# Optimization experiments

Measured on AMD Instinct MI355X. Metric: run time of the kernel, lower is better.

## Reference

```python
import jax, jax.numpy as jnp
import numpy as np

HIDDEN = 1024
N_HEADS = 16
HEAD_DIM = HIDDEN // N_HEADS


def setup_inputs() -> dict:
    key = jax.random.key(0)
    ks = jax.random.split(key, 7)
    b, l, m = 4, 1024, 1024
    q = jax.random.normal(ks[0], (b, l, HIDDEN), dtype=jnp.float32)
    k = jax.random.normal(ks[1], (b, m, HIDDEN), dtype=jnp.float32)
    v = jax.random.normal(ks[2], (b, m, HIDDEN), dtype=jnp.float32)
    s = 1.0 / np.sqrt(HIDDEN)
    w_q = jax.random.normal(ks[3], (HIDDEN, HIDDEN), dtype=jnp.float32) * s
    w_k = jax.random.normal(ks[4], (HIDDEN, HIDDEN), dtype=jnp.float32) * s
    w_v = jax.random.normal(ks[5], (HIDDEN, HIDDEN), dtype=jnp.float32) * s
    w_o = jax.random.normal(ks[6], (HIDDEN, HIDDEN), dtype=jnp.float32) * s
    return {"q": q, "k": k, "v": v, "w_q": w_q, "w_k": w_k, "w_v": w_v, "w_o": w_o}


def reference(q, k, v, w_q, w_k, w_v, w_o):
    b, l, _ = q.shape
    _, m, _ = k.shape
    # Linear (bias=False): y = x @ W^T
    qp = q @ w_q.T
    kp = k @ w_k.T
    vp = v @ w_v.T  # projected but unused downstream (faithful to original bug)
    # Faithful non-standard split: hidden -> (head_dim, n_heads)
    qh = qp.reshape(b, l, HEAD_DIM, N_HEADS)
    kh = kp.reshape(b, m, HEAD_DIM, N_HEADS)
    # attn over K, scaled, softmax over m (dim=2)
    scores = jnp.einsum('bldn,bmdn->blmn', qh, kh) / np.sqrt(HEAD_DIM)
    attn = jax.nn.softmax(scores, axis=2)
    # dropout is identity in eval mode
    # NOTE: original attends over K (not V) — reproduced faithfully
    x = jnp.einsum('blmn,bmdn->bldn', attn, kh)
    x = x.reshape(b, l, HIDDEN)  # 'b l d n -> b l (d n)'
    return x @ w_o.T
```

## Files before the change

kernel.cpp:

```cpp
#include <hip/hip_runtime.h>
#include <hip/hip_bf16.h>
#include <stdint.h>
#include <math.h>


typedef __bf16 bf16;
typedef __bf16 bf16x8 __attribute__((ext_vector_type(8)));
typedef float  f32x4  __attribute__((ext_vector_type(4)));

__device__ __forceinline__ void async_load16(const void* g, void* l) {
  __builtin_amdgcn_global_load_lds((__attribute__((address_space(1))) void*)g,
                                   (__attribute__((address_space(3))) void*)l,
                                   16, 0, 0);
}

__device__ __forceinline__ float load_canon(const void* src, int i, int fl) {
  float f = fl ? ((const float*)src)[i] : (float)((const bf16*)src)[i];
  return fminf(fmaxf(f, -1024.f), 1024.f);
}

__global__ void __launch_bounds__(256)
canon_all(const void* __restrict__ q_raw, const void* __restrict__ k_raw,
          const void* __restrict__ wq_raw, const void* __restrict__ wk_raw,
          const void* __restrict__ wo_raw,
          bf16* __restrict__ q_c, bf16* __restrict__ k_c,
          bf16* __restrict__ wq_c, bf16* __restrict__ wk_c,
          bf16* __restrict__ wo_p, int* __restrict__ flag) {
  __shared__ int smax[4];
  const int tid = threadIdx.x;
  {
    int e = (((const unsigned short*)q_raw)[tid] >> 7) & 0xFF;
#pragma unroll
    for (int off = 1; off <= 32; off <<= 1) {
      int o = __shfl_xor(e, off);
      e = o > e ? o : e;
    }
    if ((tid & 63) == 0) smax[tid >> 6] = e;
  }
  __syncthreads();
  int m01 = smax[0] > smax[1] ? smax[0] : smax[1];
  int m23 = smax[2] > smax[3] ? smax[2] : smax[3];
  const int fl = ((m01 > m23 ? m01 : m23) >= 140) ? 1 : 0;

  const int blk = blockIdx.x;
  if (blk == 0 && tid == 0) *flag = fl;

  if (blk < 4096) {
    const void* src = blk < 2048 ? q_raw : k_raw;
    bf16* dst = blk < 2048 ? q_c : k_c;
    int i = (blk & 2047) * 2048 + tid * 8;
    bf16x8 v;
#pragma unroll
    for (int j = 0; j < 8; ++j) v[j] = (bf16)load_canon(src, i + j, fl);
    *(bf16x8*)(dst + i) = v;
  } else if (blk < 5120) {
    const void* src = blk < 4608 ? wq_raw : wk_raw;
    bf16* dst = blk < 4608 ? wq_c : wk_c;
    int i = ((blk - 4096) & 511) * 2048 + tid * 8;
    bf16x8 v;
#pragma unroll
    for (int j = 0; j < 8; ++j) v[j] = (bf16)load_canon(src, i + j, fl);
    *(bf16x8*)(dst + i) = v;
  } else {
    int i = (blk - 5120) * 2048 + tid * 8;
    int o = i >> 10, h0 = i & 1023;
#pragma unroll
    for (int j = 0; j < 8; ++j) {
      int h = h0 + j;
      int kp = ((h & 15) << 6) | (h >> 4);
      wo_p[o * 1024 + kp] = (bf16)load_canon(wo_raw, i + j, fl);
    }
  }
}

__global__ void __launch_bounds__(256, 2)
qk_gemm(const bf16* __restrict__ q_c, const bf16* __restrict__ wq_c,
        const bf16* __restrict__ k_c, const bf16* __restrict__ wk_c,
        bf16* __restrict__ qh, bf16* __restrict__ kh, bf16* __restrict__ khT,
        float cs) {
  __shared__ bf16 sA[128 * 64];
  __shared__ bf16 sB[128 * 64];
  __shared__ bf16 epi[128 * 134];

  const int z = blockIdx.z;
  const bf16* A = z ? k_c : q_c;
  const bf16* W = z ? wk_c : wq_c;
  const float scale = z ? 1.0f : cs;
  bf16* out0 = z ? kh : qh;

  const int tid  = threadIdx.x;
  const int lane = tid & 63;
  const int wave = tid >> 6;
  const int q4   = lane >> 4;
  const int c16  = lane & 15;
  const int wm   = wave >> 1;
  const int wn   = wave & 1;

  const int lin    = blockIdx.x + 8 * blockIdx.y;
  const int rowBlk = (lin & 31) * 128;
  const int colBlk = (lin >> 5) * 128;

  int ar[4], ag[4];
#pragma unroll
  for (int i = 0; i < 4; ++i) {
    int s = tid + 256 * i;
    ar[i] = s >> 3;
    ag[i] = (tid & 7) ^ (ar[i] & 7);
  }
  const bf16* gA[4];
  const bf16* gB[4];
  bf16 *lA[4], *lB[4];
#pragma unroll
  for (int i = 0; i < 4; ++i) {
    gA[i] = A + (size_t)(rowBlk + ar[i]) * 1024 + ag[i] * 8;
    gB[i] = W + (size_t)(colBlk + ar[i]) * 1024 + ag[i] * 8;
    lA[i] = sA + (tid + 256 * i) * 8;
    lB[i] = sB + (tid + 256 * i) * 8;
  }

  f32x4 acc[4][4] = {};

  for (int kk = 0; kk < 1024; kk += 64) {
    __syncthreads();
#pragma unroll
    for (int i = 0; i < 4; ++i) async_load16(gA[i] + kk, lA[i]);
#pragma unroll
    for (int i = 0; i < 4; ++i) async_load16(gB[i] + kk, lB[i]);
    __builtin_amdgcn_s_waitcnt(0);
    __syncthreads();

    bf16x8 af[2][4], bfr[2][4];
#pragma unroll
    for (int ks = 0; ks < 2; ++ks) {
#pragma unroll
      for (int mt = 0; mt < 4; ++mt) {
        int row = wm * 64 + mt * 16 + c16;
        af[ks][mt] = *(const bf16x8*)(sA + row * 64 +
                       (((ks * 4 + q4) ^ (row & 7)) * 8));
      }
#pragma unroll
      for (int nt = 0; nt < 4; ++nt) {
        int row = wn * 64 + nt * 16 + c16;
        bfr[ks][nt] = *(const bf16x8*)(sB + row * 64 +
                       (((ks * 4 + q4) ^ (row & 7)) * 8));
      }
    }
#pragma unroll
    for (int ks = 0; ks < 2; ++ks)
#pragma unroll
      for (int mt = 0; mt < 4; ++mt)
#pragma unroll
        for (int nt = 0; nt < 4; ++nt)
          acc[mt][nt] = __builtin_amdgcn_mfma_f32_16x16x32_bf16(
              af[ks][mt], bfr[ks][nt], acc[mt][nt], 0, 0, 0);
  }

  __syncthreads();
#pragma unroll
  for (int mt = 0; mt < 4; ++mt)
#pragma unroll
    for (int nt = 0; nt < 4; ++nt)
#pragma unroll
      for (int r = 0; r < 4; ++r) {
        int m_t = wm * 64 + mt * 16 + q4 * 4 + r;
        int h_t = wn * 64 + nt * 16 + c16;
        epi[m_t * 134 + h_t] = (bf16)(acc[mt][nt][r] * scale);
      }
  __syncthreads();

  const int bb    = rowBlk >> 10;
  const int mbase = rowBlk & 1023;
  const int dg0   = colBlk >> 4;

  {
    int n = tid >> 4;
#pragma unroll
    for (int i = 0; i < 8; ++i) {
      int m_t = (tid & 15) + i * 16;
      bf16x8 v;
#pragma unroll
      for (int dt = 0; dt < 8; ++dt) v[dt] = epi[m_t * 134 + dt * 16 + n];
      *(bf16x8*)(out0 + ((size_t)(bb * 16 + n) * 1024 + mbase + m_t) * 64 + dg0) = v;
    }
  }
  if (z) {
    int h_t = tid >> 1, half = tid & 1;
    int n = h_t & 15, dt = h_t >> 4;
    size_t base = ((size_t)(bb * 16 + n) * 64 + dg0 + dt) * 1024 + mbase + half * 64;
#pragma unroll
    for (int c = 0; c < 8; ++c) {
      bf16x8 v;
#pragma unroll
      for (int j = 0; j < 8; ++j) v[j] = epi[(half * 64 + c * 8 + j) * 134 + h_t];
      *(bf16x8*)(khT + base + c * 8) = v;
    }
  }
}

__global__ void __launch_bounds__(256, 2)
o_gemm(const bf16* __restrict__ A, const bf16* __restrict__ W,
       bf16* __restrict__ out0, float* __restrict__ outf,
       const int* __restrict__ flag) {
  __shared__ bf16 sA[128 * 64];
  __shared__ bf16 sB[64 * 64];

  const int tid  = threadIdx.x;
  const int lane = tid & 63;
  const int wave = tid >> 6;
  const int q4   = lane >> 4;
  const int c16  = lane & 15;
  const int wm   = wave >> 1;
  const int wn   = wave & 1;

  const int lin    = blockIdx.x + 16 * blockIdx.y;
  const int rowBlk = (lin & 31) * 128;
  const int colBlk = (lin >> 5) * 64;

  int ar[4], ag[4];
#pragma unroll
  for (int i = 0; i < 4; ++i) {
    int s = tid + 256 * i;
    ar[i] = s >> 3;
    ag[i] = (tid & 7) ^ (ar[i] & 7);
  }
  const bf16* gA[4];
  bf16* lA[4];
#pragma unroll
  for (int i = 0; i < 4; ++i) {
    gA[i] = A + (size_t)(rowBlk + ar[i]) * 1024 + ag[i] * 8;
    lA[i] = sA + (tid + 256 * i) * 8;
  }
  const bf16* gB[2];
  bf16* lB[2];
#pragma unroll
  for (int i = 0; i < 2; ++i) {
    int s = tid + 256 * i;
    int br = s >> 3, bg = (tid & 7) ^ (br & 7);
    gB[i] = W + (size_t)(colBlk + br) * 1024 + bg * 8;
    lB[i] = sB + s * 8;
  }

  f32x4 acc[4][2] = {};

  for (int kk = 0; kk < 1024; kk += 64) {
    __syncthreads();
#pragma unroll
    for (int i = 0; i < 4; ++i) async_load16(gA[i] + kk, lA[i]);
#pragma unroll
    for (int i = 0; i < 2; ++i) async_load16(gB[i] + kk, lB[i]);
    __builtin_amdgcn_s_waitcnt(0);
    __syncthreads();

    bf16x8 af[2][4], bfr[2][2];
#pragma unroll
    for (int ks = 0; ks < 2; ++ks) {
#pragma unroll
      for (int mt = 0; mt < 4; ++mt) {
        int row = wm * 64 + mt * 16 + c16;
        af[ks][mt] = *(const bf16x8*)(sA + row * 64 +
                       (((ks * 4 + q4) ^ (row & 7)) * 8));
      }
#pragma unroll
      for (int nt = 0; nt < 2; ++nt) {
        int row = wn * 32 + nt * 16 + c16;
        bfr[ks][nt] = *(const bf16x8*)(sB + row * 64 +
                       (((ks * 4 + q4) ^ (row & 7)) * 8));
      }
    }
#pragma unroll
    for (int ks = 0; ks < 2; ++ks)
#pragma unroll
      for (int mt = 0; mt < 4; ++mt)
#pragma unroll
        for (int nt = 0; nt < 2; ++nt)
          acc[mt][nt] = __builtin_amdgcn_mfma_f32_16x16x32_bf16(
              af[ks][mt], bfr[ks][nt], acc[mt][nt], 0, 0, 0);
  }

  const int fl = *flag;
#pragma unroll
  for (int mt = 0; mt < 4; ++mt)
#pragma unroll
    for (int nt = 0; nt < 2; ++nt)
#pragma unroll
      for (int r = 0; r < 4; ++r) {
        int gm = rowBlk + wm * 64 + mt * 16 + q4 * 4 + r;
        int gn = colBlk + wn * 32 + nt * 16 + c16;
        size_t idx = (size_t)gm * 1024 + gn;
        if (fl) outf[idx] = acc[mt][nt][r];
        else    out0[idx] = (bf16)acc[mt][nt][r];
      }
}

__global__ void __launch_bounds__(256, 2)
attn_kernel(const bf16* __restrict__ qh, const bf16* __restrict__ kh,
            const bf16* __restrict__ khT, bf16* __restrict__ xh) {
  __shared__ bf16 sK[64 * 64];
  __shared__ bf16 sKT[64 * 64];
  __shared__ bf16 sP[4][32 * 72];

  const int tid  = threadIdx.x;
  const int lane = tid & 63;
  const int wave = tid >> 6;
  const int q4   = lane >> 4;
  const int c16  = lane & 15;
  const int bn   = blockIdx.x;
  const int b    = bn >> 4, n = bn & 15;
  const int l0w  = blockIdx.y * 128 + wave * 32;

  const bf16* qhead  = qh  + (size_t)bn * (1024 * 64);
  const bf16* khead  = kh  + (size_t)bn * (1024 * 64);
  const bf16* kThead = khT + (size_t)bn * (64 * 1024);

  bf16x8 aq[2][2];
#pragma unroll
  for (int g = 0; g < 2; ++g)
#pragma unroll
    for (int hh = 0; hh < 2; ++hh)
      aq[g][hh] = *(const bf16x8*)(qhead +
                    (size_t)(l0w + g * 16 + c16) * 64 + hh * 32 + q4 * 8);

  const int s0 = tid, s1 = tid + 256;
  const int r0 = s0 >> 3, g0 = (s0 & 7) ^ (r0 & 7);
  const int r1 = s1 >> 3, g1 = (s1 & 7) ^ (r1 & 7);

  f32x4 O[2][4] = {};
  f32x4 Osum[2] = {};
  bf16x8 ones;
#pragma unroll
  for (int j = 0; j < 8; ++j) ones[j] = (bf16)1.0f;
  bf16* sPw = sP[wave];

  for (int m0 = 0; m0 < 1024; m0 += 64) {
    __syncthreads();
    async_load16(khead + (size_t)(m0 + r0) * 64 + g0 * 8, sK + s0 * 8);
    async_load16(khead + (size_t)(m0 + r1) * 64 + g1 * 8, sK + s1 * 8);
    async_load16(kThead + (size_t)r0 * 1024 + m0 + g0 * 8, sKT + s0 * 8);
    async_load16(kThead + (size_t)r1 * 1024 + m0 + g1 * 8, sKT + s1 * 8);
    __builtin_amdgcn_s_waitcnt(0);
    __syncthreads();

    f32x4 S[2][4] = {};
#pragma unroll
    for (int t = 0; t < 4; ++t) {
#pragma unroll
      for (int hh = 0; hh < 2; ++hh) {
        int row = t * 16 + c16;
        bf16x8 bk = *(const bf16x8*)(sK + row * 64 +
                                     (((hh * 4 + q4) ^ (row & 7)) * 8));
        S[0][t] = __builtin_amdgcn_mfma_f32_16x16x32_bf16(aq[0][hh], bk, S[0][t], 0, 0, 0);
        S[1][t] = __builtin_amdgcn_mfma_f32_16x16x32_bf16(aq[1][hh], bk, S[1][t], 0, 0, 0);
      }
    }

#pragma unroll
    for (int g = 0; g < 2; ++g)
#pragma unroll
      for (int t = 0; t < 4; ++t)
#pragma unroll
        for (int r = 0; r < 4; ++r) {
          float p = exp2f(fminf(S[g][t][r], 30.0f));
          sPw[(g * 16 + q4 * 4 + r) * 72 + t * 16 + c16] = (bf16)p;
        }

    bf16x8 ap[2][2];
#pragma unroll
    for (int g = 0; g < 2; ++g) {
      ap[g][0] = *(const bf16x8*)(sPw + (g * 16 + c16) * 72 + q4 * 8);
      ap[g][1] = *(const bf16x8*)(sPw + (g * 16 + c16) * 72 + 32 + q4 * 8);
      Osum[g] = __builtin_amdgcn_mfma_f32_16x16x32_bf16(ap[g][0], ones, Osum[g], 0, 0, 0);
      Osum[g] = __builtin_amdgcn_mfma_f32_16x16x32_bf16(ap[g][1], ones, Osum[g], 0, 0, 0);
    }

#pragma unroll
    for (int td = 0; td < 4; ++td) {
#pragma unroll
      for (int hh = 0; hh < 2; ++hh) {
        int row = td * 16 + c16;
        bf16x8 bkt = *(const bf16x8*)(sKT + row * 64 +
                                      (((hh * 4 + q4) ^ (row & 7)) * 8));
        O[0][td] = __builtin_amdgcn_mfma_f32_16x16x32_bf16(ap[0][hh], bkt, O[0][td], 0, 0, 0);
        O[1][td] = __builtin_amdgcn_mfma_f32_16x16x32_bf16(ap[1][hh], bkt, O[1][td], 0, 0, 0);
      }
    }
  }

#pragma unroll
  for (int g = 0; g < 2; ++g) {
    float inv[4];
#pragma unroll
    for (int r = 0; r < 4; ++r) inv[r] = 1.0f / Osum[g][r];
#pragma unroll
    for (int td = 0; td < 4; ++td)
#pragma unroll
      for (int r = 0; r < 4; ++r)
        sPw[(g * 16 + q4 * 4 + r) * 72 + td * 16 + c16] = (bf16)(O[g][td][r] * inv[r]);
  }
  {
    int l_loc = lane >> 2, dq = lane & 3;
#pragma unroll
    for (int g = 0; g < 2; ++g) {
      bf16x8 v0 = *(const bf16x8*)(sPw + (g * 16 + l_loc) * 72 + dq * 16);
      bf16x8 v1 = *(const bf16x8*)(sPw + (g * 16 + l_loc) * 72 + dq * 16 + 8);
      size_t base = ((size_t)(b * 1024 + l0w + g * 16 + l_loc) * 16 + n) * 64 + dq * 16;
      *(bf16x8*)(xh + base)     = v0;
      *(bf16x8*)(xh + base + 8) = v1;
    }
  }
}

extern "C" void kernel_launch(void* const* d_in, const int* in_sizes, int n_in,
                              void* d_out, int out_size, void* d_ws, size_t ws_size,
                              hipStream_t stream) {
  const void* q_raw  = d_in[0];
  const void* k_raw  = d_in[1];
  const void* wq_raw = d_in[3];
  const void* wk_raw = d_in[4];
  const void* wo_raw = d_in[6];

  char* ws = (char*)d_ws;
  const size_t MB = 1024 * 1024;
  bf16* q_c  = (bf16*)(ws + 0 * MB);
  bf16* xh   = (bf16*)(ws + 0 * MB);
  bf16* k_c  = (bf16*)(ws + 8 * MB);
  bf16* kh   = (bf16*)(ws + 16 * MB);
  bf16* wq_c = (bf16*)(ws + 24 * MB);
  bf16* wk_c = (bf16*)(ws + 26 * MB);
  bf16* wo_p = (bf16*)(ws + 28 * MB);
  int*  flag = (int*)(ws + 30 * MB);
  bf16* qh   = (bf16*)d_out;
  bf16* khT  = (bf16*)((char*)d_out + 8 * MB);

  const float CS = 0.125f * 1.4426950408889634f;
  dim3 blk(256, 1, 1);

  hipLaunchKernelGGL(canon_all, dim3(5632), blk, 0, stream,
                     q_raw, k_raw, wq_raw, wk_raw, wo_raw,
                     q_c, k_c, wq_c, wk_c, wo_p, flag);
  hipLaunchKernelGGL(qk_gemm, dim3(8, 32, 2), blk, 0, stream,
                     q_c, wq_c, k_c, wk_c, qh, kh, khT, CS);
  hipLaunchKernelGGL(attn_kernel, dim3(64, 8, 1), blk, 0, stream,
                     qh, kh, khT, xh);
  hipLaunchKernelGGL(o_gemm, dim3(16, 32, 1), blk, 0, stream,
                     xh, wo_p, (bf16*)d_out, (float*)d_out, flag);
}
```

Measured before the change: 199.6 us.

## Halve tile heights and alias LDS to raise occupancy across all kernels

Measured after the change: 206.1 us. 3.2% more time.

```diff
diff --git a/kernel.cpp b/kernel.cpp
--- a/kernel.cpp
+++ b/kernel.cpp
@@ -73,14 +73,15 @@
   }
 }
 
-__global__ void __launch_bounds__(256, 2)
+__global__ void __launch_bounds__(256, 4)
 qk_gemm(const bf16* __restrict__ q_c, const bf16* __restrict__ wq_c,
         const bf16* __restrict__ k_c, const bf16* __restrict__ wk_c,
         bf16* __restrict__ qh, bf16* __restrict__ kh, bf16* __restrict__ khT,
         float cs) {
-  __shared__ bf16 sA[128 * 64];
-  __shared__ bf16 sB[128 * 64];
-  __shared__ bf16 epi[128 * 134];
+  __shared__ __attribute__((aligned(16))) char smem[24 * 1024];
+  bf16* sA  = (bf16*)smem;
+  bf16* sB  = (bf16*)(smem + 8 * 1024);
+  bf16* epi = (bf16*)smem;
 
   const int z = blockIdx.z;
   const bf16* A = z ? k_c : q_c;
@@ -97,44 +98,43 @@
   const int wn   = wave & 1;
 
   const int lin    = blockIdx.x + 8 * blockIdx.y;
-  const int rowBlk = (lin & 31) * 128;
-  const int colBlk = (lin >> 5) * 128;
-
-  int ar[4], ag[4];
+  const int rowBlk = (lin & 63) * 64;
+  const int colBlk = (lin >> 6) * 128;
+
+  const bf16* gA[2]; bf16* lA[2];
+#pragma unroll
+  for (int i = 0; i < 2; ++i) {
+    int s = tid + 256 * i;
+    int r = s >> 3, g = (s & 7) ^ (r & 7);
+    gA[i] = A + (size_t)(rowBlk + r) * 1024 + g * 8;
+    lA[i] = sA + s * 8;
+  }
+  const bf16* gB[4]; bf16* lB[4];
 #pragma unroll
   for (int i = 0; i < 4; ++i) {
     int s = tid + 256 * i;
-    ar[i] = s >> 3;
-    ag[i] = (tid & 7) ^ (ar[i] & 7);
-  }
-  const bf16* gA[4];
-  const bf16* gB[4];
-  bf16 *lA[4], *lB[4];
-#pragma unroll
-  for (int i = 0; i < 4; ++i) {
-    gA[i] = A + (size_t)(rowBlk + ar[i]) * 1024 + ag[i] * 8;
-    gB[i] = W + (size_t)(colBlk + ar[i]) * 1024 + ag[i] * 8;
-    lA[i] = sA + (tid + 256 * i) * 8;
-    lB[i] = sB + (tid + 256 * i) * 8;
-  }
-
-  f32x4 acc[4][4] = {};
+    int r = s >> 3, g = (s & 7) ^ (r & 7);
+    gB[i] = W + (size_t)(colBlk + r) * 1024 + g * 8;
+    lB[i] = sB + s * 8;
+  }
+
+  f32x4 acc[2][4] = {};
 
   for (int kk = 0; kk < 1024; kk += 64) {
     __syncthreads();
 #pragma unroll
-    for (int i = 0; i < 4; ++i) async_load16(gA[i] + kk, lA[i]);
+    for (int i = 0; i < 2; ++i) async_load16(gA[i] + kk, lA[i]);
 #pragma unroll
     for (int i = 0; i < 4; ++i) async_load16(gB[i] + kk, lB[i]);
     __builtin_amdgcn_s_waitcnt(0);
     __syncthreads();
 
-    bf16x8 af[2][4], bfr[2][4];
+    bf16x8 af[2][2], bfr[2][4];
 #pragma unroll
     for (int ks = 0; ks < 2; ++ks) {
 #pragma unroll
-      for (int mt = 0; mt < 4; ++mt) {
-        int row = wm * 64 + mt * 16 + c16;
+      for (int mt = 0; mt < 2; ++mt) {
+        int row = wm * 32 + mt * 16 + c16;
         af[ks][mt] = *(const bf16x8*)(sA + row * 64 +
                        (((ks * 4 + q4) ^ (row & 7)) * 8));
       }
@@ -148,7 +148,7 @@
 #pragma unroll
     for (int ks = 0; ks < 2; ++ks)
 #pragma unroll
-      for (int mt = 0; mt < 4; ++mt)
+      for (int mt = 0; mt < 2; ++mt)
 #pragma unroll
         for (int nt = 0; nt < 4; ++nt)
           acc[mt][nt] = __builtin_amdgcn_mfma_f32_16x16x32_bf16(
@@ -157,12 +157,12 @@
 
   __syncthreads();
 #pragma unroll
-  for (int mt = 0; mt < 4; ++mt)
+  for (int mt = 0; mt < 2; ++mt)
 #pragma unroll
     for (int nt = 0; nt < 4; ++nt)
 #pragma unroll
       for (int r = 0; r < 4; ++r) {
-        int m_t = wm * 64 + mt * 16 + q4 * 4 + r;
+        int m_t = wm * 32 + mt * 16 + q4 * 4 + r;
         int h_t = wn * 64 + nt * 16 + c16;
         epi[m_t * 134 + h_t] = (bf16)(acc[mt][nt][r] * scale);
       }
@@ -175,7 +175,7 @@
   {
     int n = tid >> 4;
 #pragma unroll
-    for (int i = 0; i < 8; ++i) {
+    for (int i = 0; i < 4; ++i) {
       int m_t = (tid & 15) + i * 16;
       bf16x8 v;
 #pragma unroll
@@ -184,24 +184,25 @@
     }
   }
   if (z) {
-    int h_t = tid >> 1, half = tid & 1;
-    int n = h_t & 15, dt = h_t >> 4;
-    size_t base = ((size_t)(bb * 16 + n) * 64 + dg0 + dt) * 1024 + mbase + half * 64;
-#pragma unroll
-    for (int c = 0; c < 8; ++c) {
+#pragma unroll
+    for (int it = 0; it < 4; ++it) {
+      int hm = tid + 256 * it;
+      int h_t = hm >> 3, c = hm & 7;
+      int n = h_t & 15, dt = h_t >> 4;
       bf16x8 v;
 #pragma unroll
-      for (int j = 0; j < 8; ++j) v[j] = epi[(half * 64 + c * 8 + j) * 134 + h_t];
-      *(bf16x8*)(khT + base + c * 8) = v;
-    }
-  }
-}
-
-__global__ void __launch_bounds__(256, 2)
+      for (int j = 0; j < 8; ++j) v[j] = epi[(c * 8 + j) * 134 + h_t];
+      *(bf16x8*)(khT + ((size_t)(bb * 16 + n) * 64 + dg0 + dt) * 1024 +
+                 mbase + c * 8) = v;
+    }
+  }
+}
+
+__global__ void __launch_bounds__(256, 4)
 o_gemm(const bf16* __restrict__ A, const bf16* __restrict__ W,
        bf16* __restrict__ out0, float* __restrict__ outf,
        const int* __restrict__ flag) {
-  __shared__ bf16 sA[128 * 64];
+  __shared__ bf16 sA[64 * 64];
   __shared__ bf16 sB[64 * 64];
 
   const int tid  = threadIdx.x;
@@ -213,50 +214,38 @@
   const int wn   = wave & 1;
 
   const int lin    = blockIdx.x + 16 * blockIdx.y;
-  const int rowBlk = (lin & 31) * 128;
-  const int colBlk = (lin >> 5) * 64;
-
-  int ar[4], ag[4];
-#pragma unroll
-  for (int i = 0; i < 4; ++i) {
-    int s = tid + 256 * i;
-    ar[i] = s >> 3;
-    ag[i] = (tid & 7) ^ (ar[i] & 7);
-  }
-  const bf16* gA[4];
-  bf16* lA[4];
-#pragma unroll
-  for (int i = 0; i < 4; ++i) {
-    gA[i] = A + (size_t)(rowBlk + ar[i]) * 1024 + ag[i] * 8;
-    lA[i] = sA + (tid + 256 * i) * 8;
-  }
-  const bf16* gB[2];
-  bf16* lB[2];
+  const int rowBlk = (lin & 63) * 64;
+  const int colBlk = (lin >> 6) * 64;
+
+  const bf16* gA[2]; bf16* lA[2];
+  const bf16* gB[2]; bf16* lB[2];
 #pragma unroll
   for (int i = 0; i < 2; ++i) {
     int s = tid + 256 * i;
-    int br = s >> 3, bg = (tid & 7) ^ (br & 7);
-    gB[i] = W + (size_t)(colBlk + br) * 1024 + bg * 8;
+    int r = s >> 3, g = (s & 7) ^ (r & 7);
+    gA[i] = A + (size_t)(rowBlk + r) * 1024 + g * 8;
+    lA[i] = sA + s * 8;
+    gB[i] = W + (size_t)(colBlk + r) * 1024 + g * 8;
     lB[i] = sB + s * 8;
   }
 
-  f32x4 acc[4][2] = {};
+  f32x4 acc[2][2] = {};
 
   for (int kk = 0; kk < 1024; kk += 64) {
     __syncthreads();
 #pragma unroll
-    for (int i = 0; i < 4; ++i) async_load16(gA[i] + kk, lA[i]);
+    for (int i = 0; i < 2; ++i) async_load16(gA[i] + kk, lA[i]);
 #pragma unroll
     for (int i = 0; i < 2; ++i) async_load16(gB[i] + kk, lB[i]);
     __builtin_amdgcn_s_waitcnt(0);
     __syncthreads();
 
-    bf16x8 af[2][4], bfr[2][2];
+    bf16x8 af[2][2], bfr[2][2];
 #pragma unroll
     for (int ks = 0; ks < 2; ++ks) {
 #pragma unroll
-      for (int mt = 0; mt < 4; ++mt) {
-        int row = wm * 64 + mt * 16 + c16;
+      for (int mt = 0; mt < 2; ++mt) {
+        int row = wm * 32 + mt * 16 + c16;
         af[ks][mt] = *(const bf16x8*)(sA + row * 64 +
                        (((ks * 4 + q4) ^ (row & 7)) * 8));
       }
@@ -270,7 +259,7 @@
 #pragma unroll
     for (int ks = 0; ks < 2; ++ks)
 #pragma unroll
-      for (int mt = 0; mt < 4; ++mt)
+      for (int mt = 0; mt < 2; ++mt)
 #pragma unroll
         for (int nt = 0; nt < 2; ++nt)
           acc[mt][nt] = __builtin_amdgcn_mfma_f32_16x16x32_bf16(
@@ -279,12 +268,12 @@
 
   const int fl = *flag;
 #pragma unroll
-  for (int mt = 0; mt < 4; ++mt)
+  for (int mt = 0; mt < 2; ++mt)
 #pragma unroll
     for (int nt = 0; nt < 2; ++nt)
 #pragma unroll
       for (int r = 0; r < 4; ++r) {
-        int gm = rowBlk + wm * 64 + mt * 16 + q4 * 4 + r;
+        int gm = rowBlk + wm * 32 + mt * 16 + q4 * 4 + r;
         int gn = colBlk + wn * 32 + nt * 16 + c16;
         size_t idx = (size_t)gm * 1024 + gn;
         if (fl) outf[idx] = acc[mt][nt][r];
@@ -292,12 +281,12 @@
       }
 }
 
-__global__ void __launch_bounds__(256, 2)
+__global__ void __launch_bounds__(256, 4)
 attn_kernel(const bf16* __restrict__ qh, const bf16* __restrict__ kh,
             const bf16* __restrict__ khT, bf16* __restrict__ xh) {
   __shared__ bf16 sK[64 * 64];
   __shared__ bf16 sKT[64 * 64];
-  __shared__ bf16 sP[4][32 * 72];
+  __shared__ bf16 sP[4][16 * 72];
 
   const int tid  = threadIdx.x;
   const int lane = tid & 63;
@@ -306,26 +295,23 @@
   const int c16  = lane & 15;
   const int bn   = blockIdx.x;
   const int b    = bn >> 4, n = bn & 15;
-  const int l0w  = blockIdx.y * 128 + wave * 32;
+  const int l0   = blockIdx.y * 64 + wave * 16;
 
   const bf16* qhead  = qh  + (size_t)bn * (1024 * 64);
   const bf16* khead  = kh  + (size_t)bn * (1024 * 64);
   const bf16* kThead = khT + (size_t)bn * (64 * 1024);
 
-  bf16x8 aq[2][2];
-#pragma unroll
-  for (int g = 0; g < 2; ++g)
-#pragma unroll
-    for (int hh = 0; hh < 2; ++hh)
-      aq[g][hh] = *(const bf16x8*)(qhead +
-                    (size_t)(l0w + g * 16 + c16) * 64 + hh * 32 + q4 * 8);
+  bf16x8 aq[2];
+#pragma unroll
+  for (int hh = 0; hh < 2; ++hh)
+    aq[hh] = *(const bf16x8*)(qhead + (size_t)(l0 + c16) * 64 + hh * 32 + q4 * 8);
 
   const int s0 = tid, s1 = tid + 256;
   const int r0 = s0 >> 3, g0 = (s0 & 7) ^ (r0 & 7);
   const int r1 = s1 >> 3, g1 = (s1 & 7) ^ (r1 & 7);
 
-  f32x4 O[2][4] = {};
-  f32x4 Osum[2] = {};
+  f32x4 O[4] = {};
+  f32x4 Osum = {};
   bf16x8 ones;
 #pragma unroll
   for (int j = 0; j < 8; ++j) ones[j] = (bf16)1.0f;
@@ -340,7 +326,7 @@
     __builtin_amdgcn_s_waitcnt(0);
     __syncthreads();
 
-    f32x4 S[2][4] = {};
+    f32x4 S[4] = {};
 #pragma unroll
     for (int t = 0; t < 4; ++t) {
 #pragma unroll
@@ -348,29 +334,23 @@
         int row = t * 16 + c16;
         bf16x8 bk = *(const bf16x8*)(sK + row * 64 +
                                      (((hh * 4 + q4) ^ (row & 7)) * 8));
-        S[0][t] = __builtin_amdgcn_mfma_f32_16x16x32_bf16(aq[0][hh], bk, S[0][t], 0, 0, 0);
-        S[1][t] = __builtin_amdgcn_mfma_f32_16x16x32_bf16(aq[1][hh], bk, S[1][t], 0, 0, 0);
-      }
-    }
-
-#pragma unroll
-    for (int g = 0; g < 2; ++g)
-#pragma unroll
-      for (int t = 0; t < 4; ++t)
-#pragma unroll
-        for (int r = 0; r < 4; ++r) {
-          float p = exp2f(fminf(S[g][t][r], 30.0f));
-          sPw[(g * 16 + q4 * 4 + r) * 72 + t * 16 + c16] = (bf16)p;
-        }
-
-    bf16x8 ap[2][2];
-#pragma unroll
-    for (int g = 0; g < 2; ++g) {
-      ap[g][0] = *(const bf16x8*)(sPw + (g * 16 + c16) * 72 + q4 * 8);
-      ap[g][1] = *(const bf16x8*)(sPw + (g * 16 + c16) * 72 + 32 + q4 * 8);
-      Osum[g] = __builtin_amdgcn_mfma_f32_16x16x32_bf16(ap[g][0], ones, Osum[g], 0, 0, 0);
-      Osum[g] = __builtin_amdgcn_mfma_f32_16x16x32_bf16(ap[g][1], ones, Osum[g], 0, 0, 0);
-    }
+        S[t] = __builtin_amdgcn_mfma_f32_16x16x32_bf16(aq[hh], bk, S[t], 0, 0, 0);
+      }
+    }
+
+#pragma unroll
+    for (int t = 0; t < 4; ++t)
+#pragma unroll
+      for (int r = 0; r < 4; ++r) {
+        float p = exp2f(fminf(S[t][r], 30.0f));
+        sPw[(q4 * 4 + r) * 72 + t * 16 + c16] = (bf16)p;
+      }
+
+    bf16x8 ap[2];
+    ap[0] = *(const bf16x8*)(sPw + c16 * 72 + q4 * 8);
+    ap[1] = *(const bf16x8*)(sPw + c16 * 72 + 32 + q4 * 8);
+    Osum = __builtin_amdgcn_mfma_f32_16x16x32_bf16(ap[0], ones, Osum, 0, 0, 0);
+    Osum = __builtin_amdgcn_mfma_f32_16x16x32_bf16(ap[1], ones, Osum, 0, 0, 0);
 
 #pragma unroll
     for (int td = 0; td < 4; ++td) {
@@ -379,33 +359,26 @@
         int row = td * 16 + c16;
         bf16x8 bkt = *(const bf16x8*)(sKT + row * 64 +
                                       (((hh * 4 + q4) ^ (row & 7)) * 8));
-        O[0][td] = __builtin_amdgcn_mfma_f32_16x16x32_bf16(ap[0][hh], bkt, O[0][td], 0, 0, 0);
-        O[1][td] = __builtin_amdgcn_mfma_f32_16x16x32_bf16(ap[1][hh], bkt, O[1][td], 0, 0, 0);
-      }
-    }
-  }
-
-#pragma unroll
-  for (int g = 0; g < 2; ++g) {
-    float inv[4];
-#pragma unroll
-    for (int r = 0; r < 4; ++r) inv[r] = 1.0f / Osum[g][r];
-#pragma unroll
-    for (int td = 0; td < 4; ++td)
-#pragma unroll
-      for (int r = 0; r < 4; ++r)
-        sPw[(g * 16 + q4 * 4 + r) * 72 + td * 16 + c16] = (bf16)(O[g][td][r] * inv[r]);
-  }
+        O[td] = __builtin_amdgcn_mfma_f32_16x16x32_bf16(ap[hh], bkt, O[td], 0, 0, 0);
+      }
+    }
+  }
+
+  float inv[4];
+#pragma unroll
+  for (int r = 0; r < 4; ++r) inv[r] = 1.0f / Osum[r];
+#pragma unroll
+  for (int td = 0; td < 4; ++td)
+#pragma unroll
+    for (int r = 0; r < 4; ++r)
+      sPw[(q4 * 4 + r) * 72 + td * 16 + c16] = (bf16)(O[td][r] * inv[r]);
   {
     int l_loc = lane >> 2, dq = lane & 3;
-#pragma unroll
-    for (int g = 0; g < 2; ++g) {
-      bf16x8 v0 = *(const bf16x8*)(sPw + (g * 16 + l_loc) * 72 + dq * 16);
-      bf16x8 v1 = *(const bf16x8*)(sPw + (g * 16 + l_loc) * 72 + dq * 16 + 8);
-      size_t base = ((size_t)(b * 1024 + l0w + g * 16 + l_loc) * 16 + n) * 64 + dq * 16;
-      *(bf16x8*)(xh + base)     = v0;
-      *(bf16x8*)(xh + base + 8) = v1;
-    }
+    bf16x8 v0 = *(const bf16x8*)(sPw + l_loc * 72 + dq * 16);
+    bf16x8 v1 = *(const bf16x8*)(sPw + l_loc * 72 + dq * 16 + 8);
+    size_t base = ((size_t)(b * 1024 + l0 + l_loc) * 16 + n) * 64 + dq * 16;
+    *(bf16x8*)(xh + base)     = v0;
+    *(bf16x8*)(xh + base + 8) = v1;
   }
 }
 
@@ -437,10 +410,10 @@
   hipLaunchKernelGGL(canon_all, dim3(5632), blk, 0, stream,
                      q_raw, k_raw, wq_raw, wk_raw, wo_raw,
                      q_c, k_c, wq_c, wk_c, wo_p, flag);
-  hipLaunchKernelGGL(qk_gemm, dim3(8, 32, 2), blk, 0, stream,
+  hipLaunchKernelGGL(qk_gemm, dim3(8, 64, 2), blk, 0, stream,
                      q_c, wq_c, k_c, wk_c, qh, kh, khT, CS);
-  hipLaunchKernelGGL(attn_kernel, dim3(64, 8, 1), blk, 0, stream,
+  hipLaunchKernelGGL(attn_kernel, dim3(64, 16, 1), blk, 0, stream,
                      qh, kh, khT, xh);
-  hipLaunchKernelGGL(o_gemm, dim3(16, 32, 1), blk, 0, stream,
+  hipLaunchKernelGGL(o_gemm, dim3(16, 64, 1), blk, 0, stream,
                      xh, wo_p, (bf16*)d_out, (float*)d_out, flag);
 }
```
